# Performance work log

Hardware: AMD Instinct MI355X
Metric: run time of the kernel (lower is better)

## Reference

```python
import jax, jax.numpy as jnp
import numpy as np

# (dy, dx) offsets corresponding to the single -1 entries of kernels 1..8
# delta1 rows: (0,0),(0,1),(0,2),(1,2); delta2 = spatial flip: (2,2),(2,1),(2,0),(1,0)
OFFSETS = [(-1, -1), (-1, 0), (-1, 1), (0, 1), (1, 1), (1, 0), (1, -1), (0, -1)]
NUM_LAYER = 9
EPS = 1e-12


def _shift(x, dy, dx):
    # zero-padded shift: out[y, x] = in[y + dy, x + dx]; dilation = shifts[0] = 1
    b, c, h, w = x.shape
    p = jnp.pad(x, ((0, 0), (0, 0), (1, 1), (1, 1)))
    return jax.lax.dynamic_slice(p, (0, 0, 1 + dy, 1 + dx), (b, c, h, w))


def _l2norm(v, axis):
    # matches torch.nn.functional.normalize: v / max(||v||, eps)
    n = jnp.sqrt(jnp.sum(v * v, axis=axis, keepdims=True))
    return v / jnp.maximum(n, EPS)


def setup_inputs() -> dict:
    key = jax.random.key(0)
    k1, k2, k3, k4 = jax.random.split(key, 4)
    B, C, H, W = 4, 256, 96, 96
    cen = jax.random.normal(k1, (B, C, H, W), dtype=jnp.float32)
    scale = 1.0 / np.sqrt(C)
    # grouped 1x1 convs (groups=9): per-group (C x C) weight matrices
    W1 = jax.random.normal(k2, (NUM_LAYER, C, C), dtype=jnp.float32) * scale
    W2 = jax.random.normal(k3, (C, C), dtype=jnp.float32) * scale
    W3 = jax.random.normal(k4, (NUM_LAYER, C, C), dtype=jnp.float32) * scale
    return {"cen": cen, "W1": W1, "W2": W2, "W3": W3}


def reference(cen, W1, W2, W3):
    b, c, h, w = cen.shape
    # Extract_layer: 8 fixed depthwise 3x3 convs (each = negated shift) + identity
    surrounds = jnp.stack(
        [-_shift(cen, dy, dx) for dy, dx in OFFSETS] + [cen], axis=1
    )  # (b, 9, c, h, w)
    # Analyze_layer: grouped 1x1 convs = per-group matmuls
    out1 = jnp.einsum("gij,bgjhw->bgihw", W1, surrounds)
    out2 = jnp.einsum("ij,bjhw->bihw", W2, cen)[:, None]  # (b, 1, c, h, w)
    out3 = jnp.einsum("gij,bgjhw->bgihw", W3, surrounds)
    out1 = _l2norm(out1, axis=2)
    out2 = _l2norm(out2, axis=2)
    out3 = _l2norm(out3, axis=2)
    # softmax over a size-1 axis (dim=2 after mean+keepdim) -> identically 1.0
    att = jax.nn.softmax(
        jnp.mean(out1 * out2, axis=2, keepdims=True), axis=2
    )  # (b, 9, 1, h, w)
    out = jnp.sum(att * out3, axis=1)  # (b, c, h, w)
    return out + cen
```

## Files before the change

### kernel.cpp

```cpp
#include <hip/hip_runtime.h>
#include <stdint.h>

#define BB 4
#define CC 256
#define HH 96
#define WW 96
#define HP 98
#define CP 264
#define XT 32
#define YT 2
#define XE 34

typedef __bf16 bf16x8 __attribute__((ext_vector_type(8)));
typedef float f32x4 __attribute__((ext_vector_type(4)));
typedef float f32x16 __attribute__((ext_vector_type(16)));

__device__ __forceinline__ uint16_t f2bf(float f) {
    uint32_t u = __float_as_uint(f);
    u += 0x7FFFu + ((u >> 16) & 1u);
    return (uint16_t)(u >> 16);
}

__global__ void zero_halo(uint16_t* __restrict__ cenT) {
    int idx = blockIdx.x * 256 + threadIdx.x;
    if (idx >= 1552 * 33) return;
    int p = idx / 33, q = idx - p * 33;
    int b = p / 388, s = p - b * 388;
    int y, x;
    if (s < 98)      { y = 0;       x = s; }
    else if (s < 196){ y = 97;      x = s - 98; }
    else if (s < 292){ x = 0;       y = s - 196 + 1; }
    else             { x = 97;      y = s - 292 + 1; }
    size_t o = (((size_t)b * HP + y) * HP + x) * CP + q * 8;
    *(uint4*)(cenT + o) = make_uint4(0u, 0u, 0u, 0u);
}

__global__ void transpose_cen(const float* __restrict__ cen, uint16_t* __restrict__ cenT) {
    const int y = blockIdx.x, b = blockIdx.y, ch = blockIdx.z, tid = threadIdx.x;
    __shared__ uint16_t ldsX[128 * 100];

    #pragma unroll
    for (int i = 0; i < 12; ++i) {
        int f = i * 256 + tid;
        int c = f / 24, xq = f % 24;
        float4 v = *(const float4*)(cen + ((((size_t)b * CC + ch * 128 + c) * HH + y) * WW + xq * 4));
        uint2 pk;
        pk.x = (uint32_t)f2bf(v.x) | ((uint32_t)f2bf(v.y) << 16);
        pk.y = (uint32_t)f2bf(v.z) | ((uint32_t)f2bf(v.w) << 16);
        *(uint2*)(&ldsX[c * 100 + xq * 4]) = pk;
    }
    __syncthreads();
    #pragma unroll
    for (int i = 0; i < 6; ++i) {
        int t = i * 256 + tid;
        int x = t % 96, cq = t / 96;
        uint32_t w0, w1, w2, w3;
        w0 = (uint32_t)ldsX[(cq * 8 + 0) * 100 + x] | ((uint32_t)ldsX[(cq * 8 + 1) * 100 + x] << 16);
        w1 = (uint32_t)ldsX[(cq * 8 + 2) * 100 + x] | ((uint32_t)ldsX[(cq * 8 + 3) * 100 + x] << 16);
        w2 = (uint32_t)ldsX[(cq * 8 + 4) * 100 + x] | ((uint32_t)ldsX[(cq * 8 + 5) * 100 + x] << 16);
        w3 = (uint32_t)ldsX[(cq * 8 + 6) * 100 + x] | ((uint32_t)ldsX[(cq * 8 + 7) * 100 + x] << 16);
        size_t o = (((size_t)b * HP + (y + 1)) * HP + (x + 1)) * CP + ch * 128 + cq * 8;
        *(uint4*)(cenT + o) = make_uint4(w0, w1, w2, w3);
    }
}

__global__ void cvt_w3(const float* __restrict__ W3, uint16_t* __restrict__ W3bf) {
    int e = (blockIdx.x * 256 + threadIdx.x) * 4;
    int g = e >> 16, n = (e >> 8) & 255, k = e & 255;
    float4 v = *(const float4*)(W3 + e);
    uint2 pk;
    pk.x = (uint32_t)f2bf(v.x) | ((uint32_t)f2bf(v.y) << 16);
    pk.y = (uint32_t)f2bf(v.z) | ((uint32_t)f2bf(v.w) << 16);
    size_t o = (size_t)(((g * 8 + (n >> 5)) * 16 + (k >> 4)) * 512)
             + (n & 31) * 16 + ((k >> 3) & 1) * 8 + (k & 7);
    *(uint2*)(W3bf + o) = pk;
}

__global__ __launch_bounds__(256, 2)
void ecm_main(const float* __restrict__ cen, const uint16_t* __restrict__ cenT,
              const uint16_t* __restrict__ W3bf, float* __restrict__ out) {
    const int tid = threadIdx.x;
    const int wv = tid >> 6, lane = tid & 63, col = lane & 31, kh = lane >> 5;
    const int x0 = blockIdx.x * XT, y0 = blockIdx.y * YT, b = blockIdx.z;

    __shared__ __align__(16) uint16_t ldsA[YT * XE * CP];
    __shared__ __align__(16) float ldsP[2][64][4];

    const int dgOrd[9] = {0, 1, 2, 7, 8, 3, 6, 5, 4};

    const uint16_t* wbA = W3bf + (size_t)(2 * wv) * (16 * 512) + col * 16 + kh * 8;
    f32x16 finA0 = {}, finA1 = {}, finB0 = {}, finB1 = {};

    #pragma unroll 1
    for (int idx = 0; idx < 9; ++idx) {
        const int g = dgOrd[idx], dg = idx / 3, dx = idx % 3 - 1;

        if (idx % 3 == 0) {
            for (int r = 0; r < YT; ++r) {
                const uint4* gs = (const uint4*)(cenT + (((size_t)b * HP + (y0 + dg + r)) * HP + x0) * CP);
                uint4* ls = (uint4*)(ldsA + r * XE * CP);
                for (int c = tid; c < XE * CP / 8; c += 256) ls[c] = gs[c];
            }
            __syncthreads();
        }

        const uint16_t* wgA = wbA + (size_t)g * 65536;
        const uint16_t* wgB = wgA + 16 * 512;
        const int a0 = (col + dx + 1) * CP + kh * 8;
        const int a1 = a0 + XE * CP;

        f32x16 aA0 = {}, aA1 = {}, aB0 = {}, aB1 = {};

        bf16x8 A0[4], A1[4], Bq0[2], Bq1[2];
        #pragma unroll
        for (int i = 0; i < 4; ++i) {
            A0[i] = *(const bf16x8*)(wgA + i * 512);
            A1[i] = *(const bf16x8*)(wgB + i * 512);
        }
        #pragma unroll
        for (int i = 0; i < 2; ++i) {
            Bq0[i] = *(const bf16x8*)(ldsA + a0 + i * 16);
            Bq1[i] = *(const bf16x8*)(ldsA + a1 + i * 16);
        }

        #pragma unroll
        for (int ks = 0; ks < 16; ++ks) {
            bf16x8 wa = A0[ks & 3], wb = A1[ks & 3];
            bf16x8 v0 = Bq0[ks & 1], v1 = Bq1[ks & 1];
            if (ks + 4 < 16) {
                A0[ks & 3] = *(const bf16x8*)(wgA + (ks + 4) * 512);
                A1[ks & 3] = *(const bf16x8*)(wgB + (ks + 4) * 512);
            }
            if (ks + 2 < 16) {
                Bq0[ks & 1] = *(const bf16x8*)(ldsA + a0 + (ks + 2) * 16);
                Bq1[ks & 1] = *(const bf16x8*)(ldsA + a1 + (ks + 2) * 16);
            }
            aA0 = __builtin_amdgcn_mfma_f32_32x32x16_bf16(wa, v0, aA0, 0, 0, 0);
            aB0 = __builtin_amdgcn_mfma_f32_32x32x16_bf16(wb, v0, aB0, 0, 0, 0);
            aA1 = __builtin_amdgcn_mfma_f32_32x32x16_bf16(wa, v1, aA1, 0, 0, 0);
            aB1 = __builtin_amdgcn_mfma_f32_32x32x16_bf16(wb, v1, aB1, 0, 0, 0);
        }

        float s0 = 0.f, s1 = 0.f;
        #pragma unroll
        for (int r = 0; r < 16; ++r) {
            s0 += aA0[r] * aA0[r] + aB0[r] * aB0[r];
            s1 += aA1[r] * aA1[r] + aB1[r] * aB1[r];
        }
        s0 += __shfl_xor(s0, 32, 64);
        s1 += __shfl_xor(s1, 32, 64);
        if (kh == 0) { ldsP[idx & 1][col][wv] = s0; ldsP[idx & 1][32 + col][wv] = s1; }
        __syncthreads();

        f32x4 pa = *(const f32x4*)&ldsP[idx & 1][col][0];
        f32x4 qa = *(const f32x4*)&ldsP[idx & 1][32 + col][0];
        float n0 = pa[0] + pa[1] + pa[2] + pa[3];
        float n1 = qa[0] + qa[1] + qa[2] + qa[3];
        const float sgn = (g == 8) ? 1.f : -1.f;
        float sc0 = sgn / fmaxf(sqrtf(n0), 1e-12f);
        float sc1 = sgn / fmaxf(sqrtf(n1), 1e-12f);
        #pragma unroll
        for (int r = 0; r < 16; ++r) {
            finA0[r] += aA0[r] * sc0; finB0[r] += aB0[r] * sc0;
            finA1[r] += aA1[r] * sc1; finB1[r] += aB1[r] * sc1;
        }
    }

    #pragma unroll
    for (int r = 0; r < 16; ++r) {
        int chA = wv * 64 + (r & 3) + 8 * (r >> 2) + 4 * kh;
        size_t oA0 = (((size_t)b * CC + chA) * HH + y0) * WW + (x0 + col);
        size_t oA1 = oA0 + WW;
        out[oA0] = finA0[r] + cen[oA0];
        out[oA1] = finA1[r] + cen[oA1];
        size_t oB0 = oA0 + (size_t)32 * HH * WW;
        size_t oB1 = oB0 + WW;
        out[oB0] = finB0[r] + cen[oB0];
        out[oB1] = finB1[r] + cen[oB1];
    }
}

extern "C" void kernel_launch(void* const* d_in, const int* in_sizes, int n_in,
                              void* d_out, int out_size, void* d_ws, size_t ws_size,
                              hipStream_t stream) {
    const float* cen = (const float*)d_in[0];
    const float* W3 = (const float*)d_in[3];
    float* out = (float*)d_out;

    uint16_t* cenT = (uint16_t*)d_ws;
    const size_t cenT_elems = (size_t)BB * HP * HP * CP;
    uint16_t* W3bf = cenT + cenT_elems;

    zero_halo<<<201, 256, 0, stream>>>(cenT);
    transpose_cen<<<dim3(HH, BB, 2), 256, 0, stream>>>(cen, cenT);
    cvt_w3<<<576, 256, 0, stream>>>(W3, W3bf);
    ecm_main<<<dim3(3, 48, 4), 256, 0, stream>>>(cen, cenT, W3bf, out);
}
```

Baseline: 195.1 us.

## Stage W3 weight tiles into LDS via async global_load_lds double buffering

Weight fragments are no longer loaded per-wave straight from global memory into registers. Each wave now issues direct global-to-LDS copies of its share of the W3 tile into a double-buffered LDS region, and the MFMA operands are then read from LDS. The W3 layout is reordered so that these 16-byte copies are contiguous per lane. The goal is to overlap weight fetches with compute and cut redundant global traffic, at the cost of about 32KB of extra LDS, which may lower occupancy, plus a __syncthreads on every k-step.

```diff
diff --git a/kernel.cpp b/kernel.cpp
--- a/kernel.cpp
+++ b/kernel.cpp
@@ -19,6 +19,12 @@
     uint32_t u = __float_as_uint(f);
     u += 0x7FFFu + ((u >> 16) & 1u);
     return (uint16_t)(u >> 16);
+}
+
+__device__ __forceinline__ void gll16(const uint16_t* g, uint16_t* l) {
+    __builtin_amdgcn_global_load_lds(
+        (const __attribute__((address_space(1))) uint32_t*)g,
+        (__attribute__((address_space(3))) uint32_t*)l, 16, 0, 0);
 }
 
 __global__ void zero_halo(uint16_t* __restrict__ cenT) {
@@ -72,7 +78,7 @@
     pk.x = (uint32_t)f2bf(v.x) | ((uint32_t)f2bf(v.y) << 16);
     pk.y = (uint32_t)f2bf(v.z) | ((uint32_t)f2bf(v.w) << 16);
     size_t o = (size_t)(((g * 8 + (n >> 5)) * 16 + (k >> 4)) * 512)
-             + (n & 31) * 16 + ((k >> 3) & 1) * 8 + (k & 7);
+             + ((k >> 3) & 1) * 256 + (n & 31) * 8 + (k & 7);
     *(uint2*)(W3bf + o) = pk;
 }
 
@@ -84,11 +90,12 @@
     const int x0 = blockIdx.x * XT, y0 = blockIdx.y * YT, b = blockIdx.z;
 
     __shared__ __align__(16) uint16_t ldsA[YT * XE * CP];
+    __shared__ __align__(16) uint16_t ldsW[2 * 16 * 512];
     __shared__ __align__(16) float ldsP[2][64][4];
 
     const int dgOrd[9] = {0, 1, 2, 7, 8, 3, 6, 5, 4};
 
-    const uint16_t* wbA = W3bf + (size_t)(2 * wv) * (16 * 512) + col * 16 + kh * 8;
+    const int fo = lane * 8;
     f32x16 finA0 = {}, finA1 = {}, finB0 = {}, finB1 = {};
 
     #pragma unroll 1
@@ -101,44 +108,49 @@
                 uint4* ls = (uint4*)(ldsA + r * XE * CP);
                 for (int c = tid; c < XE * CP / 8; c += 256) ls[c] = gs[c];
             }
-            __syncthreads();
-        }
-
-        const uint16_t* wgA = wbA + (size_t)g * 65536;
-        const uint16_t* wgB = wgA + 16 * 512;
+        }
+
+        const uint16_t* wg = W3bf + (size_t)g * 65536 + fo;
         const int a0 = (col + dx + 1) * CP + kh * 8;
         const int a1 = a0 + XE * CP;
 
+        #pragma unroll
+        for (int i = 0; i < 4; ++i) {
+            int u = wv * 4 + i, ksip = u >> 3, t = u & 7;
+            gll16(wg + ((size_t)t * 16 + ksip) * 512, ldsW + u * 512);
+        }
+
         f32x16 aA0 = {}, aA1 = {}, aB0 = {}, aB1 = {};
 
-        bf16x8 A0[4], A1[4], Bq0[2], Bq1[2];
-        #pragma unroll
-        for (int i = 0; i < 4; ++i) {
-            A0[i] = *(const bf16x8*)(wgA + i * 512);
-            A1[i] = *(const bf16x8*)(wgB + i * 512);
-        }
-        #pragma unroll
-        for (int i = 0; i < 2; ++i) {
-            Bq0[i] = *(const bf16x8*)(ldsA + a0 + i * 16);
-            Bq1[i] = *(const bf16x8*)(ldsA + a1 + i * 16);
-        }
-
-        #pragma unroll
-        for (int ks = 0; ks < 16; ++ks) {
-            bf16x8 wa = A0[ks & 3], wb = A1[ks & 3];
-            bf16x8 v0 = Bq0[ks & 1], v1 = Bq1[ks & 1];
-            if (ks + 4 < 16) {
-                A0[ks & 3] = *(const bf16x8*)(wgA + (ks + 4) * 512);
-                A1[ks & 3] = *(const bf16x8*)(wgB + (ks + 4) * 512);
+        #pragma unroll
+        for (int p = 0; p < 8; ++p) {
+            __syncthreads();
+            if (p < 7) {
+                #pragma unroll
+                for (int i = 0; i < 4; ++i) {
+                    int u = wv * 4 + i, ksip = u >> 3, t = u & 7;
+                    gll16(wg + ((size_t)t * 16 + (p + 1) * 2 + ksip) * 512,
+                          ldsW + ((p + 1) & 1) * 8192 + u * 512);
+                }
             }
-            if (ks + 2 < 16) {
-                Bq0[ks & 1] = *(const bf16x8*)(ldsA + a0 + (ks + 2) * 16);
-                Bq1[ks & 1] = *(const bf16x8*)(ldsA + a1 + (ks + 2) * 16);
-            }
-            aA0 = __builtin_amdgcn_mfma_f32_32x32x16_bf16(wa, v0, aA0, 0, 0, 0);
-            aB0 = __builtin_amdgcn_mfma_f32_32x32x16_bf16(wb, v0, aB0, 0, 0, 0);
-            aA1 = __builtin_amdgcn_mfma_f32_32x32x16_bf16(wa, v1, aA1, 0, 0, 0);
-            aB1 = __builtin_amdgcn_mfma_f32_32x32x16_bf16(wb, v1, aB1, 0, 0, 0);
+            const uint16_t* wb = ldsW + (p & 1) * 8192;
+            bf16x8 wa0k0 = *(const bf16x8*)(wb + (0 * 8 + 2 * wv) * 512 + fo);
+            bf16x8 wa1k0 = *(const bf16x8*)(wb + (0 * 8 + 2 * wv + 1) * 512 + fo);
+            bf16x8 wa0k1 = *(const bf16x8*)(wb + (1 * 8 + 2 * wv) * 512 + fo);
+            bf16x8 wa1k1 = *(const bf16x8*)(wb + (1 * 8 + 2 * wv + 1) * 512 + fo);
+            const int ko = p * 32;
+            bf16x8 b00 = *(const bf16x8*)(ldsA + a0 + ko);
+            bf16x8 b10 = *(const bf16x8*)(ldsA + a1 + ko);
+            bf16x8 b01 = *(const bf16x8*)(ldsA + a0 + ko + 16);
+            bf16x8 b11 = *(const bf16x8*)(ldsA + a1 + ko + 16);
+            aA0 = __builtin_amdgcn_mfma_f32_32x32x16_bf16(wa0k0, b00, aA0, 0, 0, 0);
+            aB0 = __builtin_amdgcn_mfma_f32_32x32x16_bf16(wa1k0, b00, aB0, 0, 0, 0);
+            aA1 = __builtin_amdgcn_mfma_f32_32x32x16_bf16(wa0k0, b10, aA1, 0, 0, 0);
+            aB1 = __builtin_amdgcn_mfma_f32_32x32x16_bf16(wa1k0, b10, aB1, 0, 0, 0);
+            aA0 = __builtin_amdgcn_mfma_f32_32x32x16_bf16(wa0k1, b01, aA0, 0, 0, 0);
+            aB0 = __builtin_amdgcn_mfma_f32_32x32x16_bf16(wa1k1, b01, aB0, 0, 0, 0);
+            aA1 = __builtin_amdgcn_mfma_f32_32x32x16_bf16(wa0k1, b11, aA1, 0, 0, 0);
+            aB1 = __builtin_amdgcn_mfma_f32_32x32x16_bf16(wa1k1, b11, aB1, 0, 0, 0);
         }
 
         float s0 = 0.f, s1 = 0.f;
```

Result: slower. 210.2 us (+7.7%).
